# Performance work log

Hardware: AMD Instinct MI355X
Metric: run time of the kernel (lower is better)

The kernel has to match this reference:

```python
import jax, jax.numpy as jnp
import numpy as np

NUM_HEAD = 8
HEAD_DIM = 64
LMK = 32          # num_landmarks
WIN = 128         # window_size
DIM = 512         # transformer_dim == num_head*head_dim
EXT = WIN // 2    # ext_len in get_tiles_v2
TILE = 2 * EXT + WIN  # 256
SCALE = 1.0 / np.sqrt(HEAD_DIM)
NEG_INF = float('-inf')


def layernorm(x, g, b, eps=1e-5):
    m = jnp.mean(x, axis=-1, keepdims=True)
    v = jnp.mean((x - m) ** 2, axis=-1, keepdims=True)
    return (x - m) * jax.lax.rsqrt(v + eps) * g + b


def split_heads(x):
    b, s, _ = x.shape
    return x.reshape(b, s, NUM_HEAD, HEAD_DIM).transpose(0, 2, 1, 3)


def setup_inputs() -> dict:
    key = jax.random.key(0)
    ks = jax.random.split(key, 8)
    B, S = 2, 8192
    w = lambda k, sh: (jax.random.normal(k, sh, jnp.float32) * 0.02)
    return {
        'X': jax.random.normal(ks[0], (B, S, DIM), jnp.float32),
        'mask': jnp.ones((B, S), jnp.bool_),
        'Wq_w': w(ks[1], (DIM, DIM)), 'Wq_b': jnp.zeros((DIM,), jnp.float32),
        'Wk_w': w(ks[2], (DIM, DIM)), 'Wk_b': jnp.zeros((DIM,), jnp.float32),
        'Wv_w': w(ks[3], (DIM, DIM)), 'Wv_b': jnp.zeros((DIM,), jnp.float32),
        'Wo_w': w(ks[4], (DIM, DIM)), 'Wo_b': jnp.zeros((DIM,), jnp.float32),
        'ln_l_g': jnp.ones((DIM,), jnp.float32), 'ln_l_b': jnp.zeros((DIM,), jnp.float32),
        'ln_s_g': jnp.ones((DIM,), jnp.float32), 'ln_s_b': jnp.zeros((DIM,), jnp.float32),
        'dconv_w': w(ks[5], (DIM, NUM_HEAD * LMK)), 'dconv_b': jnp.zeros((NUM_HEAD * LMK,), jnp.float32),
    }


def reference(X, mask, Wq_w, Wq_b, Wk_w, Wk_b, Wv_w, Wv_b, Wo_w, Wo_b,
              ln_l_g, ln_l_b, ln_s_g, ln_s_b, dconv_w, dconv_b):
    B, S, D = X.shape
    G = S // WIN  # number of window groups
    pad_mask = ~mask  # True where padded

    Q = split_heads(X @ Wq_w + Wq_b) * SCALE                       # [B,H,S,dh]
    K = split_heads(layernorm(X @ Wk_w + Wk_b, ln_l_g, ln_l_b))    # [B,H,S,dh]
    V = split_heads(layernorm(X @ Wv_w + Wv_b, ln_l_g, ln_l_b))    # [B,H,S,dh]

    # --- landmark (long-range) compression ---
    hs = X @ dconv_w + dconv_b                                     # [B,S,H*L]
    hs = jnp.where(pad_mask[:, :, None], NEG_INF, hs)
    hs = jax.nn.softmax(hs.astype(jnp.float32), axis=1).astype(X.dtype)
    hs = hs.reshape(B, S, NUM_HEAD, LMK).transpose(0, 2, 3, 1)     # [B,H,L,S]
    K_c = jnp.einsum('bhls,bhsd->bhld', hs, K)                     # [B,H,L,dh]
    V_c = jnp.einsum('bhls,bhsd->bhld', hs, V)
    # dual LayerNorm on compressed keys/values (over combined head dim)
    K_c = split_heads(layernorm(K_c.transpose(0, 2, 1, 3).reshape(B, LMK, D), ln_s_g, ln_s_b))
    V_c = split_heads(layernorm(V_c.transpose(0, 2, 1, 3).reshape(B, LMK, D), ln_s_g, ln_s_b))

    attn_compress = jnp.einsum('bhsd,bhld->bhsl', Q, K_c)          # [B,H,S,L]

    # --- sliding-window (short-range) scores, v2 tiling ---
    idx = jnp.arange(G)[:, None] * WIN + jnp.arange(TILE)[None, :]  # [G,TILE] indices into padded seq
    K_pad = jnp.pad(K, ((0, 0), (0, 0), (EXT, EXT), (0, 0)))
    K_tiles = K_pad[:, :, idx, :]                                   # [B,H,G,TILE,dh]
    mask_pad = jnp.pad(pad_mask, ((0, 0), (EXT, EXT)), constant_values=True)
    mask_tiles = mask_pad[:, idx]                                   # [B,G,TILE]
    Q_tiles = Q.reshape(B, NUM_HEAD, G, WIN, HEAD_DIM)
    win = jnp.einsum('bhgwd,bhgtd->bhgwt', Q_tiles, K_tiles)
    win = jnp.where(mask_tiles[:, None, :, None, :], NEG_INF, win)
    win = win.reshape(B, NUM_HEAD, S, TILE)

    # --- joint softmax over [landmarks | window] ---
    all_scores = jnp.concatenate([attn_compress, win], axis=-1)     # [B,H,S,L+TILE]
    probs = jax.nn.softmax(all_scores.astype(jnp.float32), axis=-1).astype(X.dtype)
    probs = jnp.where(pad_mask[:, None, :, None], 0.0, probs)

    C = jnp.einsum('bhsl,bhld->bhsd', probs[..., :LMK], V_c)        # landmark contribution
    win_p = probs[..., LMK:].reshape(B, NUM_HEAD, G, WIN, TILE)
    V_pad = jnp.pad(V, ((0, 0), (0, 0), (EXT, EXT), (0, 0)))
    V_tiles = V_pad[:, :, idx, :]                                   # [B,H,G,TILE,dh]
    C = C + jnp.einsum('bhgwt,bhgtd->bhgwd', win_p, V_tiles).reshape(B, NUM_HEAD, S, HEAD_DIM)

    out = C.transpose(0, 2, 1, 3).reshape(B, S, D) @ Wo_w + Wo_b
    return out
```

## Files before the change

### kernel.cpp

```cpp
#include <hip/hip_runtime.h>

typedef unsigned short u16;
typedef unsigned int u32;
typedef __attribute__((ext_vector_type(8))) short bf16x8;
typedef __attribute__((ext_vector_type(4))) float f32x4;

#define DEVI static __device__ __forceinline__

DEVI float bf2f(u16 u){ u32 x = ((u32)u) << 16; float f; __builtin_memcpy(&f, &x, 4); return f; }
DEVI u16 f2bf(float f){ u32 x; __builtin_memcpy(&x, &f, 4); u32 r = x + 0x7FFFu + ((x >> 16) & 1u); return (u16)(r >> 16); }
DEVI u32 pk2(float a, float b){ return ((u32)f2bf(b) << 16) | (u32)f2bf(a); }

DEVI f32x4 mfma16(bf16x8 a, bf16x8 b, f32x4 c){
  return __builtin_amdgcn_mfma_f32_16x16x32_bf16(a, b, c, 0, 0, 0);
}

typedef __attribute__((address_space(3))) u32* lds_ptr_t;
typedef const __attribute__((address_space(1))) u32* gbl_ptr_t;
DEVI void gload16(const void* g, const void* l){
  __builtin_amdgcn_global_load_lds((gbl_ptr_t)(unsigned long long)g,
                                   (lds_ptr_t)(unsigned long long)l,
                                   16, 0, 0);
}

__global__ void cvt_x_kernel(const float* __restrict__ X, u16* __restrict__ Xb){
  int i = blockIdx.x * 256 + threadIdx.x;
  const f32x4* p = (const f32x4*)X;
  f32x4 a = p[(size_t)i*2], c = p[(size_t)i*2 + 1];
  bf16x8 v;
  v[0]=(short)f2bf(a[0]); v[1]=(short)f2bf(a[1]); v[2]=(short)f2bf(a[2]); v[3]=(short)f2bf(a[3]);
  v[4]=(short)f2bf(c[0]); v[5]=(short)f2bf(c[1]); v[6]=(short)f2bf(c[2]); v[7]=(short)f2bf(c[3]);
  *(bf16x8*)(Xb + (size_t)i*8) = v;
}

__global__ void transpose_all(const float* __restrict__ Wq, const float* __restrict__ Wk,
                              const float* __restrict__ Wv, const float* __restrict__ Wd,
                              const float* __restrict__ Wo,
                              const float* __restrict__ Wqb, const float* __restrict__ Wkb,
                              const float* __restrict__ Wvb, const float* __restrict__ Wdb,
                              u16* __restrict__ WT, float* __restrict__ biasAll)
{
  int id = blockIdx.x;
  if (id >= 1152){
    int c = (id - 1152) * 256 + threadIdx.x;
    float v = (c < 512) ? Wqb[c] : (c < 1024) ? Wkb[c-512] : (c < 1536) ? Wvb[c-1024] : Wdb[c-1536];
    biasAll[c] = v;
    return;
  }
  const float* W; int RO, N, local;
  if      (id < 256){ W = Wq; RO = 0;    N = 512; local = id; }
  else if (id < 512){ W = Wk; RO = 512;  N = 512; local = id - 256; }
  else if (id < 768){ W = Wv; RO = 1024; N = 512; local = id - 512; }
  else if (id < 896){ W = Wd; RO = 1536; N = 256; local = id - 768; }
  else              { W = Wo; RO = 1792; N = 512; local = id - 896; }
  int ntiles = N >> 5;
  int n0 = (local & (ntiles - 1)) * 32, k0 = (local / ntiles) * 32;
  __shared__ float tile[32][33];
  int tx = threadIdx.x & 31, ty = threadIdx.x >> 5;
  #pragma unroll
  for (int i = 0; i < 32; i += 8)
    tile[ty + i][tx] = W[(size_t)(k0 + ty + i) * N + n0 + tx];
  __syncthreads();
  #pragma unroll
  for (int i = 0; i < 32; i += 8)
    WT[(size_t)(RO + n0 + ty + i) * 512 + k0 + tx] = f2bf(tile[tx][ty + i]);
}

__global__ __launch_bounds__(256) void gemm_qkvh(
    const u16* __restrict__ Xb, const u16* __restrict__ WT, const float* __restrict__ biasAll,
    u16* __restrict__ Qb, u16* __restrict__ Kb, u16* __restrict__ Vb,
    float* __restrict__ hsf, float* __restrict__ cmx, float* __restrict__ csm)
{
  __shared__ __align__(16) u16 As[128*32];
  __shared__ __align__(16) u16 Bs[128*32];
  __shared__ float pm[2][128], ps[2][128];
  const int t = threadIdx.x, lane = t & 63, w = t >> 6;
  const int m0 = blockIdx.y * 128, n0 = blockIdx.x * 128;
  const int wr = (w >> 1) * 64, wc = (w & 1) * 64;
  const int lrow = lane & 15, lk = lane >> 4;
  const f32x4 fz = {0.f, 0.f, 0.f, 0.f};
  f32x4 acc[4][4];
  #pragma unroll
  for (int mi = 0; mi < 4; mi++)
    #pragma unroll
    for (int ni = 0; ni < 4; ni++) acc[mi][ni] = fz;

  for (int k0 = 0; k0 < 512; k0 += 32){
    #pragma unroll
    for (int r = 0; r < 2; r++){
      int idx = r*256 + t;
      int row = idx >> 2;
      int kc  = (idx & 3) ^ (row & 3);
      gload16(Xb + (size_t)(m0+row)*512 + k0 + kc*8, (const void*)(As + r*2048 + w*512));
      gload16(WT + (size_t)(n0+row)*512 + k0 + kc*8, (const void*)(Bs + r*2048 + w*512));
    }
    __syncthreads();
    bf16x8 af[4], bfv[4];
    #pragma unroll
    for (int i = 0; i < 4; i++){
      int ra = wr + i*16 + lrow;
      af[i]  = *(const bf16x8*)(As + ra*32 + ((lk ^ (ra & 3)) * 8));
      int rb = wc + i*16 + lrow;
      bfv[i] = *(const bf16x8*)(Bs + rb*32 + ((lk ^ (rb & 3)) * 8));
    }
    #pragma unroll
    for (int mi = 0; mi < 4; mi++)
      #pragma unroll
      for (int ni = 0; ni < 4; ni++)
        acc[mi][ni] = mfma16(af[mi], bfv[ni], acc[mi][ni]);
    __syncthreads();
  }

  const int sel = blockIdx.x >> 2;
  if (sel < 3){
    u16* dst = (sel == 0) ? Qb : (sel == 1) ? Kb : Vb;
    const float scale = (sel == 0) ? 0.125f : 1.0f;
    #pragma unroll
    for (int mi = 0; mi < 4; mi++){
      #pragma unroll
      for (int ni = 0; ni < 4; ni++){
        int gcol = n0 + wc + ni*16 + lrow;
        int lcol = gcol & 511;
        float bv = biasAll[gcol];
        int hh = lcol >> 6, d = lcol & 63;
        #pragma unroll
        for (int r = 0; r < 4; r++){
          int grow = m0 + wr + mi*16 + lk*4 + r;
          int b = grow >> 13, s = grow & 8191;
          float v = (acc[mi][ni][r] + bv) * scale;
          dst[(((size_t)(b*8 + hh))*8192 + s)*64 + d] = f2bf(v);
        }
      }
    }
  } else {
    float mx[4], sm[4];
    #pragma unroll
    for (int ni = 0; ni < 4; ni++){ mx[ni] = -1e30f; sm[ni] = 0.f; }
    #pragma unroll
    for (int ni = 0; ni < 4; ni++){
      int gcol = n0 + wc + ni*16 + lrow;
      float bv = biasAll[gcol];
      int c = gcol - 1536;
      #pragma unroll
      for (int mi = 0; mi < 4; mi++){
        #pragma unroll
        for (int r = 0; r < 4; r++){
          int grow = m0 + wr + mi*16 + lk*4 + r;
          float v = acc[mi][ni][r] + bv;
          hsf[(size_t)grow*256 + c] = v;
          float nm = fmaxf(mx[ni], v);
          sm[ni] = sm[ni]*__expf(mx[ni]-nm) + __expf(v-nm);
          mx[ni] = nm;
        }
      }
    }
    #pragma unroll
    for (int ni = 0; ni < 4; ni++){
      #pragma unroll
      for (int d2 = 16; d2 <= 32; d2 <<= 1){
        float om = __shfl_xor(mx[ni], d2);
        float os = __shfl_xor(sm[ni], d2);
        float nm = fmaxf(mx[ni], om);
        sm[ni] = sm[ni]*__expf(mx[ni]-nm) + os*__expf(om-nm);
        mx[ni] = nm;
      }
    }
    if (lk == 0){
      #pragma unroll
      for (int ni = 0; ni < 4; ni++){
        pm[wr >> 6][wc + ni*16 + lrow] = mx[ni];
        ps[wr >> 6][wc + ni*16 + lrow] = sm[ni];
      }
    }
    __syncthreads();
    if (t < 128){
      float ma = pm[0][t], mb = pm[1][t];
      float nm = fmaxf(ma, mb);
      float s = ps[0][t]*__expf(ma-nm) + ps[1][t]*__expf(mb-nm);
      int b = m0 >> 13, chunk = (m0 & 8191) >> 7;
      int c = (n0 - 1536) + t;
      cmx[((size_t)b*64 + chunk)*256 + c] = nm;
      csm[((size_t)b*64 + chunk)*256 + c] = s;
    }
  }
}

__global__ __launch_bounds__(256) void gemm_out(
    const u16* __restrict__ A, const u16* __restrict__ Bt,
    const float* __restrict__ bias, float* __restrict__ Cf)
{
  __shared__ __align__(16) u16 As[128*32];
  __shared__ __align__(16) u16 Bs[128*32];
  const int t = threadIdx.x, lane = t & 63, w = t >> 6;
  const int m0 = blockIdx.y * 128, n0 = blockIdx.x * 128;
  const int wr = (w >> 1) * 64, wc = (w & 1) * 64;
  const int lrow = lane & 15, lk = lane >> 4;
  const f32x4 fz = {0.f, 0.f, 0.f, 0.f};
  f32x4 acc[4][4];
  #pragma unroll
  for (int mi = 0; mi < 4; mi++)
    #pragma unroll
    for (int ni = 0; ni < 4; ni++) acc[mi][ni] = fz;

  for (int k0 = 0; k0 < 512; k0 += 32){
    #pragma unroll
    for (int r = 0; r < 2; r++){
      int idx = r*256 + t;
      int row = idx >> 2;
      int kc  = (idx & 3) ^ (row & 3);
      gload16(A  + (size_t)(m0+row)*512 + k0 + kc*8, (const void*)(As + r*2048 + w*512));
      gload16(Bt + (size_t)(n0+row)*512 + k0 + kc*8, (const void*)(Bs + r*2048 + w*512));
    }
    __syncthreads();
    bf16x8 af[4], bfv[4];
    #pragma unroll
    for (int i = 0; i < 4; i++){
      int ra = wr + i*16 + lrow;
      af[i]  = *(const bf16x8*)(As + ra*32 + ((lk ^ (ra & 3)) * 8));
      int rb = wc + i*16 + lrow;
      bfv[i] = *(const bf16x8*)(Bs + rb*32 + ((lk ^ (rb & 3)) * 8));
    }
    #pragma unroll
    for (int mi = 0; mi < 4; mi++)
      #pragma unroll
      for (int ni = 0; ni < 4; ni++)
        acc[mi][ni] = mfma16(af[mi], bfv[ni], acc[mi][ni]);
    __syncthreads();
  }

  #pragma unroll
  for (int mi = 0; mi < 4; mi++){
    #pragma unroll
    for (int ni = 0; ni < 4; ni++){
      int gcol = n0 + wc + ni*16 + lrow;
      float bv = bias[gcol];
      #pragma unroll
      for (int r = 0; r < 4; r++){
        int grow = m0 + wr + mi*16 + lk*4 + r;
        Cf[(size_t)grow * 512 + gcol] = acc[mi][ni][r] + bv;
      }
    }
  }
}

__global__ __launch_bounds__(256) void ln_both(u16* __restrict__ Kb, u16* __restrict__ Vb,
    const float* __restrict__ gg, const float* __restrict__ bb)
{
  u16* buf = blockIdx.y ? Vb : Kb;
  const int lane = threadIdx.x & 63, w = threadIdx.x >> 6;
  const int row = blockIdx.x * 4 + w;
  const int b = row >> 13, si = row & 8191;
  const int hh = lane >> 3, d = (lane & 7) * 8;
  u16* p = buf + (((size_t)(b*8 + hh))*8192 + si)*64 + d;
  bf16x8 raw = *(const bf16x8*)p;
  float x[8];
  #pragma unroll
  for (int j = 0; j < 8; j++) x[j] = bf2f((u16)raw[j]);
  float s = 0.f, q = 0.f;
  #pragma unroll
  for (int j = 0; j < 8; j++){ s += x[j]; q += x[j]*x[j]; }
  #pragma unroll
  for (int d2 = 1; d2 < 64; d2 <<= 1){ s += __shfl_xor(s, d2); q += __shfl_xor(q, d2); }
  float mean = s * (1.f/512.f);
  float var  = q * (1.f/512.f) - mean*mean;
  float rstd = rsqrtf(var + 1e-5f);
  int c0 = lane * 8;
  bf16x8 o;
  #pragma unroll
  for (int j = 0; j < 8; j++)
    o[j] = (short)f2bf((x[j] - mean) * rstd * gg[c0+j] + bb[c0+j]);
  *(bf16x8*)p = o;
}

__global__ __launch_bounds__(256) void transpose_v(const u16* __restrict__ Vb, u16* __restrict__ VbT){
  __shared__ u16 tile[64][72];
  const int st = blockIdx.x, bh = blockIdx.y;
  const int t = threadIdx.x;
  {
    int row = t >> 2, cc = (t & 3) * 16;
    const u16* src = Vb + ((size_t)bh*8192 + st*64 + row)*64 + cc;
    *(bf16x8*)&tile[row][cc]     = *(const bf16x8*)src;
    *(bf16x8*)&tile[row][cc + 8] = *(const bf16x8*)(src + 8);
  }
  __syncthreads();
  {
    int d = t >> 2, sc4 = (t & 3) * 16;
    bf16x8 o0, o1;
    #pragma unroll
    for (int i = 0; i < 8; i++) o0[i] = (short)tile[sc4 + i][d];
    #pragma unroll
    for (int i = 0; i < 8; i++) o1[i] = (short)tile[sc4 + 8 + i][d];
    u16* dst = VbT + ((size_t)bh*64 + d)*8192 + st*64 + sc4;
    *(bf16x8*)dst       = o0;
    *(bf16x8*)(dst + 8) = o1;
  }
}

__global__ void smax_comb(const float* __restrict__ cmax, const float* __restrict__ csum,
                          float* __restrict__ gmax, float* __restrict__ gsum){
  int b = blockIdx.x, c = threadIdx.x;
  float m = -1e30f, s = 0.f;
  for (int ch = 0; ch < 64; ch++){
    float cm = cmax[((size_t)b*64 + ch)*256 + c];
    float cs = csum[((size_t)b*64 + ch)*256 + c];
    float nm = fmaxf(m, cm);
    s = s*__expf(m - nm) + cs*__expf(cm - nm);
    m = nm;
  }
  gmax[b*256 + c] = m; gsum[b*256 + c] = s;
}

__global__ __launch_bounds__(256) void cmp_accum(const float* __restrict__ hsf,
    const float* __restrict__ gmax, const float* __restrict__ gsum,
    const u16* __restrict__ Kb, const u16* __restrict__ Vb,
    float* __restrict__ pK, float* __restrict__ pV)
{
  __shared__ float Pls[64*36];
  __shared__ __align__(16) float Klf[64*68];
  __shared__ __align__(16) float Vlf[64*68];
  const int sch = blockIdx.x, bh = blockIdx.y;
  const int b = bh >> 3, h = bh & 7;
  const int t = threadIdx.x;
  const int l = t >> 3, d0 = (t & 7) * 8;
  const int c0 = (t & 3) * 8;
  float gm[8], gi[8];
  #pragma unroll
  for (int j = 0; j < 8; j++){
    int c = h*32 + c0 + j;
    gm[j] = gmax[b*256 + c];
    gi[j] = 1.0f / gsum[b*256 + c];
  }
  float aK[8], aV[8];
  #pragma unroll
  for (int j = 0; j < 8; j++){ aK[j] = 0.f; aV[j] = 0.f; }

  for (int sub = 0; sub < 4; sub++){
    int s0 = sch*256 + sub*64;
    {
      int row = t >> 2;
      const float* src = hsf + ((size_t)b*8192 + s0 + row)*256 + h*32 + c0;
      f32x4 x0 = *(const f32x4*)src, x1 = *(const f32x4*)(src + 4);
      #pragma unroll
      for (int j = 0; j < 4; j++){
        Pls[row*36 + c0 + j]     = __expf(x0[j] - gm[j])   * gi[j];
        Pls[row*36 + c0 + 4 + j] = __expf(x1[j] - gm[4+j]) * gi[4+j];
      }
    }
    {
      int row = t >> 2, e0 = (t & 3) * 16;
      const u16* ks = Kb + ((size_t)bh*8192 + s0 + row)*64 + e0;
      const u16* vs = Vb + ((size_t)bh*8192 + s0 + row)*64 + e0;
      bf16x8 k0 = *(const bf16x8*)ks, k1 = *(const bf16x8*)(ks + 8);
      bf16x8 v0 = *(const bf16x8*)vs, v1 = *(const bf16x8*)(vs + 8);
      #pragma unroll
      for (int j = 0; j < 8; j++){
        Klf[row*68 + e0 + j]     = bf2f((u16)k0[j]);
        Klf[row*68 + e0 + 8 + j] = bf2f((u16)k1[j]);
        Vlf[row*68 + e0 + j]     = bf2f((u16)v0[j]);
        Vlf[row*68 + e0 + 8 + j] = bf2f((u16)v1[j]);
      }
    }
    __syncthreads();
    #pragma unroll 2
    for (int si = 0; si < 64; si++){
      float p = Pls[si*36 + l];
      f32x4 ka = *(const f32x4*)&Klf[si*68 + d0];
      f32x4 kb = *(const f32x4*)&Klf[si*68 + d0 + 4];
      f32x4 va = *(const f32x4*)&Vlf[si*68 + d0];
      f32x4 vb = *(const f32x4*)&Vlf[si*68 + d0 + 4];
      #pragma unroll
      for (int j = 0; j < 4; j++){
        aK[j]   += p * ka[j];
        aK[4+j] += p * kb[j];
        aV[j]   += p * va[j];
        aV[4+j] += p * vb[j];
      }
    }
    __syncthreads();
  }
  size_t base = ((size_t)bh*32 + sch)*2048 + l*64 + d0;
  #pragma unroll
  for (int j = 0; j < 8; j++){ pK[base + j] = aK[j]; pV[base + j] = aV[j]; }
}

__global__ __launch_bounds__(256) void ln_c_kernel(const float* __restrict__ pK, const float* __restrict__ pV,
    const float* __restrict__ gg, const float* __restrict__ bb,
    u16* __restrict__ Kcb, u16* __restrict__ VcT)
{
  __shared__ float red[4][4];
  const int b = blockIdx.x >> 5, l = blockIdx.x & 31;
  const int t = threadIdx.x, lane = t & 63, w = t >> 6;
  float xk[2], xv[2];
  #pragma unroll
  for (int q2 = 0; q2 < 2; q2++){
    int c = t + q2*256;
    int hh = c >> 6, d = c & 63;
    float sk = 0.f, sv = 0.f;
    for (int ch = 0; ch < 32; ch++){
      size_t idx = (((size_t)(b*8 + hh)*32 + ch)*2048) + l*64 + d;
      sk += pK[idx]; sv += pV[idx];
    }
    xk[q2] = sk; xv[q2] = sv;
  }
  float s1 = xk[0]+xk[1], q1 = xk[0]*xk[0]+xk[1]*xk[1];
  float s2 = xv[0]+xv[1], q2s = xv[0]*xv[0]+xv[1]*xv[1];
  #pragma unroll
  for (int d2 = 1; d2 < 64; d2 <<= 1){
    s1 += __shfl_xor(s1, d2); q1 += __shfl_xor(q1, d2);
    s2 += __shfl_xor(s2, d2); q2s += __shfl_xor(q2s, d2);
  }
  if (lane == 0){ red[0][w]=s1; red[1][w]=q1; red[2][w]=s2; red[3][w]=q2s; }
  __syncthreads();
  s1 = red[0][0]+red[0][1]+red[0][2]+red[0][3];
  q1 = red[1][0]+red[1][1]+red[1][2]+red[1][3];
  s2 = red[2][0]+red[2][1]+red[2][2]+red[2][3];
  q2s = red[3][0]+red[3][1]+red[3][2]+red[3][3];
  float mk = s1*(1.f/512.f), vk = q1*(1.f/512.f) - mk*mk, rk = rsqrtf(vk + 1e-5f);
  float mv = s2*(1.f/512.f), vvv = q2s*(1.f/512.f) - mv*mv, rv = rsqrtf(vvv + 1e-5f);
  #pragma unroll
  for (int q2 = 0; q2 < 2; q2++){
    int c = t + q2*256;
    int hh = c >> 6, d = c & 63;
    Kcb[(((size_t)(b*8 + hh))*32 + l)*64 + d] = f2bf((xk[q2]-mk)*rk*gg[c] + bb[c]);
    VcT[(((size_t)(b*8 + hh))*64 + d)*32 + l] = f2bf((xv[q2]-mv)*rv*gg[c] + bb[c]);
  }
}

__global__ __launch_bounds__(512, 4) void attn2_kernel(
    const u16* __restrict__ Qb, const u16* __restrict__ Kb, const u16* __restrict__ Kcb,
    const u16* __restrict__ VbT, const u16* __restrict__ VcT, u16* __restrict__ Cb)
{
  __shared__ __align__(16) char smem[74752];
  u16* Vt = (u16*)(smem + 36864);
  u16* Pl = (u16*)smem;

  const int g = blockIdx.x, h = blockIdx.y, b = blockIdx.z;
  const int bh = b*8 + h;
  const int t = threadIdx.x, lane = t & 63, w = t >> 6;
  const int lrow = lane & 15, lk = lane >> 4;
  const int s0 = g*128 - 64;
  const bf16x8 bz = {0,0,0,0,0,0,0,0};
  const f32x4 fz = {0.f,0.f,0.f,0.f};

  #pragma unroll
  for (int it = 0; it < 5; it++){
    int idx = it*512 + t;
    if (idx < 2304){
      int row = idx >> 3, kc = idx & 7;
      bf16x8 v = bz;
      if (row < 256){
        int sk = s0 + row;
        if (sk >= 0 && sk < 8192) v = *(const bf16x8*)(Kb + ((size_t)bh*8192 + sk)*64 + kc*8);
      } else {
        v = *(const bf16x8*)(Kcb + ((size_t)bh*32 + (row - 256))*64 + kc*8);
      }
      int off = row*128 + kc*16; off ^= (row & 7) << 4;
      *(bf16x8*)(smem + off) = v;
    }
  }
  #pragma unroll
  for (int it = 0; it < 4; it++){
    int idx = it*512 + t;
    int d = idx >> 5, cc = idx & 31;
    int sk = s0 + cc*8;
    bf16x8 v = bz;
    if (sk >= 0 && sk < 8192) v = *(const bf16x8*)(VbT + ((size_t)bh*64 + d)*8192 + sk);
    *(bf16x8*)(Vt + d*296 + cc*8) = v;
  }
  if (t < 256){
    int d = t >> 2, cc = t & 3;
    bf16x8 v = *(const bf16x8*)(VcT + ((size_t)bh*64 + d)*32 + cc*8);
    *(bf16x8*)(Vt + d*296 + 256 + cc*8) = v;
  }
  bf16x8 qf[2];
  #pragma unroll
  for (int ks = 0; ks < 2; ks++)
    qf[ks] = *(const bf16x8*)(Qb + ((size_t)bh*8192 + g*128 + w*16 + lrow)*64 + ks*32 + lk*8);

  __syncthreads();

  f32x4 sc[18];
  #pragma unroll
  for (int j = 0; j < 18; j++) sc[j] = fz;
  #pragma unroll
  for (int j = 0; j < 18; j++){
    int row = j*16 + lrow;
    #pragma unroll
    for (int ks = 0; ks < 2; ks++){
      int off = row*128 + ks*64 + lk*16; off ^= (row & 7) << 4;
      bf16x8 kf = *(const bf16x8*)(smem + off);
      sc[j] = mfma16(kf, qf[ks], sc[j]);
    }
  }

  #pragma unroll
  for (int j = 0; j < 16; j++){
    int sb = s0 + j*16 + lk*4;
    if (sb < 0 || sb >= 8192){
      sc[j][0] = -1e30f; sc[j][1] = -1e30f; sc[j][2] = -1e30f; sc[j][3] = -1e30f;
    }
  }

  float m = -1e30f;
  #pragma unroll
  for (int j = 0; j < 18; j++)
    m = fmaxf(m, fmaxf(fmaxf(sc[j][0], sc[j][1]), fmaxf(sc[j][2], sc[j][3])));
  m = fmaxf(m, __shfl_xor(m, 16));
  m = fmaxf(m, __shfl_xor(m, 32));
  float ssum = 0.f;
  #pragma unroll
  for (int j = 0; j < 18; j++){
    #pragma unroll
    for (int r = 0; r < 4; r++){
      float e = __expf(sc[j][r] - m);
      sc[j][r] = e; ssum += e;
    }
  }
  ssum += __shfl_xor(ssum, 16);
  ssum += __shfl_xor(ssum, 32);
  float inv = 1.0f / ssum;

  f32x4 ao[4];
  #pragma unroll
  for (int nj = 0; nj < 4; nj++) ao[nj] = fz;
  const int prow = w*16 + lrow;

  #pragma unroll
  for (int c = 0; c < 3; c++){
    __syncthreads();
    #pragma unroll
    for (int jj = 0; jj < 6; jj++){
      int j = c*6 + jj;
      u32* dst = (u32*)(Pl + prow*104 + jj*16 + lk*4);
      dst[0] = pk2(sc[j][0], sc[j][1]);
      dst[1] = pk2(sc[j][2], sc[j][3]);
    }
    __syncthreads();
    #pragma unroll
    for (int ksl = 0; ksl < 3; ksl++){
      bf16x8 pb = *(const bf16x8*)(Pl + prow*104 + ksl*32 + lk*8);
      #pragma unroll
      for (int nj = 0; nj < 4; nj++){
        bf16x8 av = *(const bf16x8*)(Vt + (nj*16 + lrow)*296 + c*96 + ksl*32 + lk*8);
        ao[nj] = mfma16(av, pb, ao[nj]);
      }
    }
  }

  const int qglob = g*128 + w*16 + lrow;
  #pragma unroll
  for (int nj = 0; nj < 4; nj++){
    u32* dst = (u32*)(Cb + ((size_t)b*8192 + qglob)*512 + h*64 + nj*16 + lk*4);
    dst[0] = pk2(ao[nj][0]*inv, ao[nj][1]*inv);
    dst[1] = pk2(ao[nj][2]*inv, ao[nj][3]*inv);
  }
}

constexpr size_t OFF_XB   = 0;
constexpr size_t OFF_WT   = OFF_XB  + 16777216;
constexpr size_t OFF_QB   = OFF_WT  + 2359296;
constexpr size_t OFF_KB   = OFF_QB  + 16777216;
constexpr size_t OFF_VB   = OFF_KB  + 16777216;
constexpr size_t OFF_CB   = OFF_VB  + 16777216;
constexpr size_t OFF_VBT  = OFF_CB  + 16777216;
constexpr size_t OFF_HSF  = OFF_VBT + 16777216;
constexpr size_t OFF_CMX  = OFF_HSF + 16777216;
constexpr size_t OFF_CSM  = OFF_CMX + 131072;
constexpr size_t OFF_GMX  = OFF_CSM + 131072;
constexpr size_t OFF_GSM  = OFF_GMX + 2048;
constexpr size_t OFF_PK   = OFF_GSM + 2048;
constexpr size_t OFF_PV   = OFF_PK  + 4194304;
constexpr size_t OFF_KCB  = OFF_PV  + 4194304;
constexpr size_t OFF_VCT  = OFF_KCB + 65536;
constexpr size_t OFF_BIAS = OFF_VCT + 65536;

extern "C" void kernel_launch(void* const* d_in, const int* in_sizes, int n_in,
                              void* d_out, int out_size, void* d_ws, size_t ws_size,
                              hipStream_t stream)
{
  const float* X    = (const float*)d_in[0];
  const float* Wq   = (const float*)d_in[2];
  const float* Wqb  = (const float*)d_in[3];
  const float* Wk   = (const float*)d_in[4];
  const float* Wkb  = (const float*)d_in[5];
  const float* Wv   = (const float*)d_in[6];
  const float* Wvb  = (const float*)d_in[7];
  const float* Wo   = (const float*)d_in[8];
  const float* Wob  = (const float*)d_in[9];
  const float* lnlg = (const float*)d_in[10];
  const float* lnlb = (const float*)d_in[11];
  const float* lnsg = (const float*)d_in[12];
  const float* lnsb = (const float*)d_in[13];
  const float* Wd   = (const float*)d_in[14];
  const float* Wdb  = (const float*)d_in[15];
  float* out = (float*)d_out;

  char* ws = (char*)d_ws;
  u16*   Xb   = (u16*)(ws + OFF_XB);
  u16*   WT   = (u16*)(ws + OFF_WT);
  u16*   Qb   = (u16*)(ws + OFF_QB);
  u16*   Kb   = (u16*)(ws + OFF_KB);
  u16*   Vb   = (u16*)(ws + OFF_VB);
  u16*   Cbp  = (u16*)(ws + OFF_CB);
  u16*   VbT  = (u16*)(ws + OFF_VBT);
  float* hsf  = (float*)(ws + OFF_HSF);
  float* cmx  = (float*)(ws + OFF_CMX);
  float* csm  = (float*)(ws + OFF_CSM);
  float* gmx  = (float*)(ws + OFF_GMX);
  float* gsm  = (float*)(ws + OFF_GSM);
  float* pK   = (float*)(ws + OFF_PK);
  float* pV   = (float*)(ws + OFF_PV);
  u16*   Kcb  = (u16*)(ws + OFF_KCB);
  u16*   VcT  = (u16*)(ws + OFF_VCT);
  float* biasAll = (float*)(ws + OFF_BIAS);

  cvt_x_kernel<<<dim3(4096), dim3(256), 0, stream>>>(X, Xb);
  transpose_all<<<dim3(1159), dim3(256), 0, stream>>>(Wq, Wk, Wv, Wd, Wo,
                                                      Wqb, Wkb, Wvb, Wdb, WT, biasAll);

  gemm_qkvh<<<dim3(14,128), dim3(256), 0, stream>>>(Xb, WT, biasAll, Qb, Kb, Vb, hsf, cmx, csm);

  ln_both<<<dim3(4096,2), dim3(256), 0, stream>>>(Kb, Vb, lnlg, lnlb);
  transpose_v<<<dim3(128,16), dim3(256), 0, stream>>>(Vb, VbT);

  smax_comb<<<dim3(2), dim3(256), 0, stream>>>(cmx, csm, gmx, gsm);

  cmp_accum<<<dim3(32,16), dim3(256), 0, stream>>>(hsf, gmx, gsm, Kb, Vb, pK, pV);
  ln_c_kernel<<<dim3(64), dim3(256), 0, stream>>>(pK, pV, lnsg, lnsb, Kcb, VcT);

  attn2_kernel<<<dim3(64,8,2), dim3(512), 0, stream>>>(Qb, Kb, Kcb, VbT, VcT, Cbp);

  gemm_out<<<dim3(4,128), dim3(256), 0, stream>>>(Cbp, WT + (size_t)1792*512, Wob, out);
}
```

Measured before the change: 198.5 us.

## Fuse V layernorm stats into GEMM epilogue, MFMA landmark accumulation, XCD-aware block mapping

The QKV GEMM epilogue now emits per-row partial sum and sum-of-squares for the V projection. The V layernorm is applied on the fly inside the V transpose kernel and the landmark accumulation kernel, which removes the separate in-place V normalization pass. The landmark compression accumulation is rewritten to use bf16 MFMA on LDS-transposed tiles instead of scalar fp32 FMA loops. Both GEMMs remap 1D block ids so neighbouring M tiles land on the same XCD for L2 reuse, and the softmax combine loop is split into four independent chains. Precision drops to bf16 for the probability and V operands in the landmark accumulation, and the variance is computed as E[x^2]-mean^2.

```diff
diff --git a/kernel.cpp b/kernel.cpp
--- a/kernel.cpp
+++ b/kernel.cpp
@@ -69,13 +69,18 @@
 __global__ __launch_bounds__(256) void gemm_qkvh(
     const u16* __restrict__ Xb, const u16* __restrict__ WT, const float* __restrict__ biasAll,
     u16* __restrict__ Qb, u16* __restrict__ Kb, u16* __restrict__ Vb,
-    float* __restrict__ hsf, float* __restrict__ cmx, float* __restrict__ csm)
+    float* __restrict__ hsf, float* __restrict__ cmx, float* __restrict__ csm,
+    float* __restrict__ pstatV)
 {
   __shared__ __align__(16) u16 As[128*32];
   __shared__ __align__(16) u16 Bs[128*32];
   __shared__ float pm[2][128], ps[2][128];
+  __shared__ float vps[128][2], vqs[128][2];
+  const int bid = blockIdx.x;
+  const int xcd = bid & 7, cch = bid >> 3;
+  const int by = xcd*16 + cch/14, bx = cch % 14;
   const int t = threadIdx.x, lane = t & 63, w = t >> 6;
-  const int m0 = blockIdx.y * 128, n0 = blockIdx.x * 128;
+  const int m0 = by * 128, n0 = bx * 128;
   const int wr = (w >> 1) * 64, wc = (w & 1) * 64;
   const int lrow = lane & 15, lk = lane >> 4;
   const f32x4 fz = {0.f, 0.f, 0.f, 0.f};
@@ -111,7 +116,7 @@
     __syncthreads();
   }
 
-  const int sel = blockIdx.x >> 2;
+  const int sel = bx >> 2;
   if (sel < 3){
     u16* dst = (sel == 0) ? Qb : (sel == 1) ? Kb : Vb;
     const float scale = (sel == 0) ? 0.125f : 1.0f;
@@ -132,6 +137,35 @@
         }
       }
     }
+    if (sel == 2){
+      float bvv[4];
+      #pragma unroll
+      for (int ni = 0; ni < 4; ni++) bvv[ni] = biasAll[n0 + wc + ni*16 + lrow];
+      #pragma unroll
+      for (int mi = 0; mi < 4; mi++){
+        #pragma unroll
+        for (int r = 0; r < 4; r++){
+          float s = 0.f, q = 0.f;
+          #pragma unroll
+          for (int ni = 0; ni < 4; ni++){
+            float v = acc[mi][ni][r] + bvv[ni];
+            s += v; q += v*v;
+          }
+          #pragma unroll
+          for (int d2 = 1; d2 < 16; d2 <<= 1){ s += __shfl_xor(s, d2); q += __shfl_xor(q, d2); }
+          if (lrow == 0){
+            int rloc = wr + mi*16 + lk*4 + r;
+            vps[rloc][w & 1] = s; vqs[rloc][w & 1] = q;
+          }
+        }
+      }
+      __syncthreads();
+      if (t < 128){
+        float s = vps[t][0] + vps[t][1], q = vqs[t][0] + vqs[t][1];
+        size_t o = (size_t)(m0 + t)*8 + (bx - 8)*2;
+        pstatV[o] = s; pstatV[o + 1] = q;
+      }
+    }
   } else {
     float mx[4], sm[4];
     #pragma unroll
@@ -191,8 +225,11 @@
 {
   __shared__ __align__(16) u16 As[128*32];
   __shared__ __align__(16) u16 Bs[128*32];
+  const int bid = blockIdx.x;
+  const int xcd = bid & 7, cch = bid >> 3;
+  const int by = xcd*16 + (cch >> 2), bx = cch & 3;
   const int t = threadIdx.x, lane = t & 63, w = t >> 6;
-  const int m0 = blockIdx.y * 128, n0 = blockIdx.x * 128;
+  const int m0 = by * 128, n0 = bx * 128;
   const int wr = (w >> 1) * 64, wc = (w & 1) * 64;
   const int lrow = lane & 15, lk = lane >> 4;
   const f32x4 fz = {0.f, 0.f, 0.f, 0.f};
@@ -243,15 +280,14 @@
   }
 }
 
-__global__ __launch_bounds__(256) void ln_both(u16* __restrict__ Kb, u16* __restrict__ Vb,
+__global__ __launch_bounds__(256) void ln_k(u16* __restrict__ Kb,
     const float* __restrict__ gg, const float* __restrict__ bb)
 {
-  u16* buf = blockIdx.y ? Vb : Kb;
   const int lane = threadIdx.x & 63, w = threadIdx.x >> 6;
   const int row = blockIdx.x * 4 + w;
   const int b = row >> 13, si = row & 8191;
   const int hh = lane >> 3, d = (lane & 7) * 8;
-  u16* p = buf + (((size_t)(b*8 + hh))*8192 + si)*64 + d;
+  u16* p = Kb + (((size_t)(b*8 + hh))*8192 + si)*64 + d;
   bf16x8 raw = *(const bf16x8*)p;
   float x[8];
   #pragma unroll
@@ -272,15 +308,31 @@
   *(bf16x8*)p = o;
 }
 
-__global__ __launch_bounds__(256) void transpose_v(const u16* __restrict__ Vb, u16* __restrict__ VbT){
+__global__ __launch_bounds__(256) void transpose_ln_v(const u16* __restrict__ Vb,
+    const float* __restrict__ pstatV, const float* __restrict__ gg, const float* __restrict__ bb,
+    u16* __restrict__ VbT)
+{
   __shared__ u16 tile[64][72];
   const int st = blockIdx.x, bh = blockIdx.y;
+  const int b = bh >> 3, h = bh & 7;
   const int t = threadIdx.x;
   {
     int row = t >> 2, cc = (t & 3) * 16;
+    int grow = b*8192 + st*64 + row;
+    f32x4 p0 = *(const f32x4*)(pstatV + (size_t)grow*8);
+    f32x4 p1 = *(const f32x4*)(pstatV + (size_t)grow*8 + 4);
+    float mean = (p0[0]+p0[2]+p1[0]+p1[2]) * (1.f/512.f);
+    float msq  = (p0[1]+p0[3]+p1[1]+p1[3]) * (1.f/512.f);
+    float rstd = rsqrtf(msq - mean*mean + 1e-5f);
     const u16* src = Vb + ((size_t)bh*8192 + st*64 + row)*64 + cc;
-    *(bf16x8*)&tile[row][cc]     = *(const bf16x8*)src;
-    *(bf16x8*)&tile[row][cc + 8] = *(const bf16x8*)(src + 8);
+    bf16x8 v0 = *(const bf16x8*)src, v1 = *(const bf16x8*)(src + 8);
+    #pragma unroll
+    for (int j = 0; j < 8; j++){
+      int c = h*64 + cc + j;
+      tile[row][cc + j]     = f2bf((bf2f((u16)v0[j]) - mean)*rstd*gg[c] + bb[c]);
+      int c2 = c + 8;
+      tile[row][cc + 8 + j] = f2bf((bf2f((u16)v1[j]) - mean)*rstd*gg[c2] + bb[c2]);
+    }
   }
   __syncthreads();
   {
@@ -299,88 +351,118 @@
 __global__ void smax_comb(const float* __restrict__ cmax, const float* __restrict__ csum,
                           float* __restrict__ gmax, float* __restrict__ gsum){
   int b = blockIdx.x, c = threadIdx.x;
-  float m = -1e30f, s = 0.f;
-  for (int ch = 0; ch < 64; ch++){
-    float cm = cmax[((size_t)b*64 + ch)*256 + c];
-    float cs = csum[((size_t)b*64 + ch)*256 + c];
-    float nm = fmaxf(m, cm);
-    s = s*__expf(m - nm) + cs*__expf(cm - nm);
-    m = nm;
-  }
-  gmax[b*256 + c] = m; gsum[b*256 + c] = s;
-}
-
-__global__ __launch_bounds__(256) void cmp_accum(const float* __restrict__ hsf,
+  float m[4], s[4];
+  #pragma unroll
+  for (int u = 0; u < 4; u++){ m[u] = -1e30f; s[u] = 0.f; }
+  for (int ch = 0; ch < 64; ch += 4){
+    #pragma unroll
+    for (int u = 0; u < 4; u++){
+      float cm = cmax[((size_t)b*64 + ch + u)*256 + c];
+      float cs = csum[((size_t)b*64 + ch + u)*256 + c];
+      float nm = fmaxf(m[u], cm);
+      s[u] = s[u]*__expf(m[u] - nm) + cs*__expf(cm - nm);
+      m[u] = nm;
+    }
+  }
+  #pragma unroll
+  for (int u = 1; u < 4; u++){
+    float nm = fmaxf(m[0], m[u]);
+    s[0] = s[0]*__expf(m[0]-nm) + s[u]*__expf(m[u]-nm);
+    m[0] = nm;
+  }
+  gmax[b*256 + c] = m[0]; gsum[b*256 + c] = s[0];
+}
+
+__global__ __launch_bounds__(256) void cmp2_kernel(const float* __restrict__ hsf,
     const float* __restrict__ gmax, const float* __restrict__ gsum,
     const u16* __restrict__ Kb, const u16* __restrict__ Vb,
+    const float* __restrict__ pstatV, const float* __restrict__ gg, const float* __restrict__ bb,
     float* __restrict__ pK, float* __restrict__ pV)
 {
-  __shared__ float Pls[64*36];
-  __shared__ __align__(16) float Klf[64*68];
-  __shared__ __align__(16) float Vlf[64*68];
+  __shared__ __align__(16) u16 Pt[32*72];
+  __shared__ __align__(16) u16 Kt[64*72];
+  __shared__ __align__(16) u16 Vt[64*72];
   const int sch = blockIdx.x, bh = blockIdx.y;
   const int b = bh >> 3, h = bh & 7;
-  const int t = threadIdx.x;
-  const int l = t >> 3, d0 = (t & 7) * 8;
-  const int c0 = (t & 3) * 8;
+  const int t = threadIdx.x, lane = t & 63, w = t >> 6;
+  const int lrow = lane & 15, lk = lane >> 4;
+  const int sl = lane;
   float gm[8], gi[8];
   #pragma unroll
   for (int j = 0; j < 8; j++){
-    int c = h*32 + c0 + j;
+    int c = h*32 + w*8 + j;
     gm[j] = gmax[b*256 + c];
     gi[j] = 1.0f / gsum[b*256 + c];
   }
-  float aK[8], aV[8];
-  #pragma unroll
-  for (int j = 0; j < 8; j++){ aK[j] = 0.f; aV[j] = 0.f; }
-
-  for (int sub = 0; sub < 4; sub++){
-    int s0 = sch*256 + sub*64;
+  float glv[16], blv[16];
+  #pragma unroll
+  for (int j = 0; j < 16; j++){
+    int c = h*64 + w*16 + j;
+    glv[j] = gg[c]; blv[j] = bb[c];
+  }
+  const f32x4 fz = {0.f,0.f,0.f,0.f};
+  f32x4 aK[2], aV[2];
+  aK[0]=fz; aK[1]=fz; aV[0]=fz; aV[1]=fz;
+
+  for (int tile = 0; tile < 4; ++tile){
+    int s0 = sch*256 + tile*64;
+    int grow = b*8192 + s0 + sl;
     {
-      int row = t >> 2;
-      const float* src = hsf + ((size_t)b*8192 + s0 + row)*256 + h*32 + c0;
+      const float* src = hsf + (size_t)grow*256 + h*32 + w*8;
       f32x4 x0 = *(const f32x4*)src, x1 = *(const f32x4*)(src + 4);
       #pragma unroll
       for (int j = 0; j < 4; j++){
-        Pls[row*36 + c0 + j]     = __expf(x0[j] - gm[j])   * gi[j];
-        Pls[row*36 + c0 + 4 + j] = __expf(x1[j] - gm[4+j]) * gi[4+j];
+        Pt[(w*8 + j)*72 + sl]     = f2bf(__expf(x0[j] - gm[j])   * gi[j]);
+        Pt[(w*8 + 4 + j)*72 + sl] = f2bf(__expf(x1[j] - gm[4+j]) * gi[4+j]);
       }
     }
     {
-      int row = t >> 2, e0 = (t & 3) * 16;
-      const u16* ks = Kb + ((size_t)bh*8192 + s0 + row)*64 + e0;
-      const u16* vs = Vb + ((size_t)bh*8192 + s0 + row)*64 + e0;
+      const u16* ks = Kb + ((size_t)bh*8192 + s0 + sl)*64 + w*16;
       bf16x8 k0 = *(const bf16x8*)ks, k1 = *(const bf16x8*)(ks + 8);
+      #pragma unroll
+      for (int j = 0; j < 8; j++){
+        Kt[(w*16 + j)*72 + sl]     = (u16)k0[j];
+        Kt[(w*16 + 8 + j)*72 + sl] = (u16)k1[j];
+      }
+    }
+    {
+      f32x4 p0 = *(const f32x4*)(pstatV + (size_t)grow*8);
+      f32x4 p1 = *(const f32x4*)(pstatV + (size_t)grow*8 + 4);
+      float mean = (p0[0]+p0[2]+p1[0]+p1[2]) * (1.f/512.f);
+      float msq  = (p0[1]+p0[3]+p1[1]+p1[3]) * (1.f/512.f);
+      float rstd = rsqrtf(msq - mean*mean + 1e-5f);
+      const u16* vs = Vb + ((size_t)bh*8192 + s0 + sl)*64 + w*16;
       bf16x8 v0 = *(const bf16x8*)vs, v1 = *(const bf16x8*)(vs + 8);
       #pragma unroll
       for (int j = 0; j < 8; j++){
-        Klf[row*68 + e0 + j]     = bf2f((u16)k0[j]);
-        Klf[row*68 + e0 + 8 + j] = bf2f((u16)k1[j]);
-        Vlf[row*68 + e0 + j]     = bf2f((u16)v0[j]);
-        Vlf[row*68 + e0 + 8 + j] = bf2f((u16)v1[j]);
-      }
-    }
-    __syncthreads();
-    #pragma unroll 2
-    for (int si = 0; si < 64; si++){
-      float p = Pls[si*36 + l];
-      f32x4 ka = *(const f32x4*)&Klf[si*68 + d0];
-      f32x4 kb = *(const f32x4*)&Klf[si*68 + d0 + 4];
-      f32x4 va = *(const f32x4*)&Vlf[si*68 + d0];
-      f32x4 vb = *(const f32x4*)&Vlf[si*68 + d0 + 4];
-      #pragma unroll
-      for (int j = 0; j < 4; j++){
-        aK[j]   += p * ka[j];
-        aK[4+j] += p * kb[j];
-        aV[j]   += p * va[j];
-        aV[4+j] += p * vb[j];
-      }
-    }
-    __syncthreads();
-  }
-  size_t base = ((size_t)bh*32 + sch)*2048 + l*64 + d0;
-  #pragma unroll
-  for (int j = 0; j < 8; j++){ pK[base + j] = aK[j]; pV[base + j] = aV[j]; }
+        Vt[(w*16 + j)*72 + sl]     = f2bf((bf2f((u16)v0[j]) - mean)*rstd*glv[j]   + blv[j]);
+        Vt[(w*16 + 8 + j)*72 + sl] = f2bf((bf2f((u16)v1[j]) - mean)*rstd*glv[8+j] + blv[8+j]);
+      }
+    }
+    __syncthreads();
+    #pragma unroll
+    for (int ks = 0; ks < 2; ks++){
+      bf16x8 a0 = *(const bf16x8*)(Pt + (lrow)*72      + ks*32 + lk*8);
+      bf16x8 a1 = *(const bf16x8*)(Pt + (16 + lrow)*72 + ks*32 + lk*8);
+      bf16x8 bK = *(const bf16x8*)(Kt + (w*16 + lrow)*72 + ks*32 + lk*8);
+      bf16x8 bV = *(const bf16x8*)(Vt + (w*16 + lrow)*72 + ks*32 + lk*8);
+      aK[0] = mfma16(a0, bK, aK[0]);
+      aK[1] = mfma16(a1, bK, aK[1]);
+      aV[0] = mfma16(a0, bV, aV[0]);
+      aV[1] = mfma16(a1, bV, aV[1]);
+    }
+    __syncthreads();
+  }
+  size_t base = ((size_t)bh*32 + sch)*2048;
+  #pragma unroll
+  for (int li = 0; li < 2; li++){
+    #pragma unroll
+    for (int r = 0; r < 4; r++){
+      size_t o = base + (size_t)(li*16 + lk*4 + r)*64 + w*16 + lrow;
+      pK[o] = aK[li][r];
+      pV[o] = aV[li][r];
+    }
+  }
 }
 
 __global__ __launch_bounds__(256) void ln_c_kernel(const float* __restrict__ pK, const float* __restrict__ pV,
@@ -573,6 +655,7 @@
 constexpr size_t OFF_KCB  = OFF_PV  + 4194304;
 constexpr size_t OFF_VCT  = OFF_KCB + 65536;
 constexpr size_t OFF_BIAS = OFF_VCT + 65536;
+constexpr size_t OFF_PSV  = OFF_BIAS + 8192;
 
 extern "C" void kernel_launch(void* const* d_in, const int* in_sizes, int n_in,
                               void* d_out, int out_size, void* d_ws, size_t ws_size,
@@ -613,22 +696,25 @@
   u16*   Kcb  = (u16*)(ws + OFF_KCB);
   u16*   VcT  = (u16*)(ws + OFF_VCT);
   float* biasAll = (float*)(ws + OFF_BIAS);
+  float* pstatV  = (float*)(ws + OFF_PSV);
 
   cvt_x_kernel<<<dim3(4096), dim3(256), 0, stream>>>(X, Xb);
   transpose_all<<<dim3(1159), dim3(256), 0, stream>>>(Wq, Wk, Wv, Wd, Wo,
                                                       Wqb, Wkb, Wvb, Wdb, WT, biasAll);
 
-  gemm_qkvh<<<dim3(14,128), dim3(256), 0, stream>>>(Xb, WT, biasAll, Qb, Kb, Vb, hsf, cmx, csm);
-
-  ln_both<<<dim3(4096,2), dim3(256), 0, stream>>>(Kb, Vb, lnlg, lnlb);
-  transpose_v<<<dim3(128,16), dim3(256), 0, stream>>>(Vb, VbT);
+  gemm_qkvh<<<dim3(1792), dim3(256), 0, stream>>>(Xb, WT, biasAll, Qb, Kb, Vb,
+                                                  hsf, cmx, csm, pstatV);
+
+  ln_k<<<dim3(4096), dim3(256), 0, stream>>>(Kb, lnlg, lnlb);
+  transpose_ln_v<<<dim3(128,16), dim3(256), 0, stream>>>(Vb, pstatV, lnlg, lnlb, VbT);
 
   smax_comb<<<dim3(2), dim3(256), 0, stream>>>(cmx, csm, gmx, gsm);
 
-  cmp_accum<<<dim3(32,16), dim3(256), 0, stream>>>(hsf, gmx, gsm, Kb, Vb, pK, pV);
+  cmp2_kernel<<<dim3(32,16), dim3(256), 0, stream>>>(hsf, gmx, gsm, Kb, Vb, pstatV,
+                                                     lnlg, lnlb, pK, pV);
   ln_c_kernel<<<dim3(64), dim3(256), 0, stream>>>(pK, pV, lnsg, lnsb, Kcb, VcT);
 
   attn2_kernel<<<dim3(64,8,2), dim3(512), 0, stream>>>(Qb, Kb, Kcb, VbT, VcT, Cbp);
 
-  gemm_out<<<dim3(4,128), dim3(256), 0, stream>>>(Cbp, WT + (size_t)1792*512, Wob, out);
-}
+  gemm_out<<<dim3(512), dim3(256), 0, stream>>>(Cbp, WT + (size_t)1792*512, Wob, out);
+}
```

After: 176.8 us. 10.9% less time.
